# Optimization experiments

Measured on AMD Instinct MI355X. Metric: run time of the kernel, lower is better.

## Reference

```python
import jax, jax.numpy as jnp
import numpy as np

N_NODES = 100000
N_EDGES = 1600000
N_GRAPHS = 64
D = 128


def gcn_conv(x, W, b, src, dst, num_nodes):
    # PyG GCNConv: x' = D^{-1/2} (A + I) D^{-1/2} (X W) + b
    h = x @ W  # [N, H]
    deg = jax.ops.segment_sum(jnp.ones_like(dst, dtype=h.dtype), dst,
                              num_segments=num_nodes)  # includes self-loop (>=1)
    dinv = jax.lax.rsqrt(deg)
    norm = dinv[src] * dinv[dst]  # [E+N]
    msg = h[src] * norm[:, None]  # gather + scale
    out = jax.ops.segment_sum(msg, dst, num_segments=num_nodes)
    return out + b


def setup_inputs() -> dict:
    key = jax.random.key(0)
    ks = jax.random.split(key, 10)
    x = jax.random.normal(ks[0], (N_NODES, D), dtype=jnp.float32)
    edge_index = jax.random.randint(ks[1], (2, N_EDGES), 0, N_NODES, dtype=jnp.int64)
    batch = jnp.sort(jax.random.randint(ks[2], (N_NODES,), 0, N_GRAPHS, dtype=jnp.int64))
    s = 1.0 / np.sqrt(D)
    W1 = jax.random.normal(ks[3], (D, D), dtype=jnp.float32) * s
    b1 = jnp.zeros((D,), dtype=jnp.float32)
    W2 = jax.random.normal(ks[4], (D, D), dtype=jnp.float32) * s
    b2 = jnp.zeros((D,), dtype=jnp.float32)
    Wfc = jax.random.normal(ks[5], (D, D), dtype=jnp.float32) * s
    bfc = jnp.zeros((D,), dtype=jnp.float32)
    return {"x": x, "edge_index": edge_index, "batch": batch,
            "W1": W1, "b1": b1, "W2": W2, "b2": b2, "Wfc": Wfc, "bfc": bfc}


def reference(x, edge_index, batch, W1, b1, W2, b2, Wfc, bfc):
    num_nodes = x.shape[0]
    # add self-loops (PyG default add_self_loops=True)
    loop = jnp.arange(num_nodes, dtype=edge_index.dtype)
    src = jnp.concatenate([edge_index[0], loop])
    dst = jnp.concatenate([edge_index[1], loop])

    h = jax.nn.relu(gcn_conv(x, W1, b1, src, dst, num_nodes))
    h = jax.nn.relu(gcn_conv(h, W2, b2, src, dst, num_nodes))

    # global_mean_pool over graph segment ids
    sums = jax.ops.segment_sum(h, batch, num_segments=N_GRAPHS)
    cnts = jax.ops.segment_sum(jnp.ones((num_nodes,), h.dtype), batch,
                               num_segments=N_GRAPHS)
    pooled = sums / jnp.maximum(cnts, 1.0)[:, None]

    return jax.nn.relu(pooled @ Wfc + bfc)
```

## Files before the change

### kernel.cpp

```cpp
#include <hip/hip_runtime.h>
#include <hip/hip_bf16.h>
#include <stdint.h>

typedef unsigned int uint;
typedef unsigned short ushort;
typedef __attribute__((ext_vector_type(8))) short short8;
typedef __attribute__((ext_vector_type(4))) float floatx4;

#define DD 128
#define BSHIFT 9
#define NBLK 256
#define CAP 10240

__device__ __forceinline__ float bf2f(ushort h){ return __uint_as_float(((uint)h)<<16); }
__device__ __forceinline__ ushort f2bf(float f){
    uint u = __float_as_uint(f);
    u += 0x7fffu + ((u>>16)&1u);
    return (ushort)(u>>16);
}

__global__ __launch_bounds__(256) void k_canon2(
    const int* __restrict__ ei, const ushort* __restrict__ xs,
    const void* W1, const void* W2, const void* Wfc,
    const void* b1, const void* b2, const void* bfc,
    float* Wcf, float* bc1, float* bc2, float* bcf,
    ushort* wb1, ushort* wb2,
    int* flags, float* pooled, int* bukcnt, int nbuk, int PM)
{
    __shared__ int s_flg[3];
    int t = threadIdx.x, b = blockIdx.x;
    if (t < 64){
        unsigned long long m0 = __ballot((t < 32) ? (ei[2*t+1] == 0) : 1);
        uint ex2 = (((uint)xs[2*t]) >> 7) & 0xffu;
        uint ew2 = (((uint)((const ushort*)W1)[2*t]) >> 7) & 0xffu;
        unsigned long long m1 = __ballot(ex2 >= 90u && ex2 <= 160u);
        unsigned long long m2 = __ballot(ew2 >= 90u && ew2 <= 160u);
        if (t == 0){
            s_flg[0] = (m0 == ~0ull) ? 1 : 0;
            s_flg[1] = (__popcll(m1) >= 48) ? 1 : 0;
            s_flg[2] = (__popcll(m2) >= 48) ? 1 : 0;
            if (b == 0){ flags[0]=s_flg[0]; flags[1]=s_flg[1]; flags[2]=s_flg[2]; }
        }
    }
    __syncthreads();
    int fW = s_flg[2];

    int gi = b*256 + t;
    if (gi < 32768){
        int r = gi >> 14, off = gi & 16383;
        const void* s = (r==0) ? W1 : W2;
        float val = fW ? bf2f(((const ushort*)s)[off]) : ((const float*)s)[off];
        int k = off>>7, n = off&127;
        int c = n>>4, nn = n&15, kk = k>>5, q = (k>>3)&3, j = k&7;
        ushort* wb = (r==0) ? wb1 : wb2;
        wb[((c*4+kk)*64 + q*16 + nn)*8 + j] = f2bf(val);
    } else if (gi < 49152){
        int off = gi - 32768;
        Wcf[off] = fW ? bf2f(((const ushort*)Wfc)[off]) : ((const float*)Wfc)[off];
    } else if (gi < 49536){
        int jj = gi - 49152; int r = jj>>7, off = jj & 127;
        const void* s = (r==0)?b1:((r==1)?b2:bfc);
        float* d = (r==0)?bc1:((r==1)?bc2:bcf);
        d[off] = fW ? bf2f(((const ushort*)s)[off]) : ((const float*)s)[off];
    } else if (gi < 49536 + PM){
        pooled[gi - 49536] = 0.f;
    } else if (gi < 49536 + PM + nbuk){
        bukcnt[gi - 49536 - PM] = 0;
    }
}

__global__ __launch_bounds__(256) void k_scatA(const int* __restrict__ ei,
                                               int* __restrict__ bukcnt,
                                               uint2* __restrict__ pairs,
                                               int E, int nbuk, int chunk){
    __shared__ int lh[256], lcur[256];
    __shared__ int s_flg;
    int t = threadIdx.x, b = blockIdx.x;
    if (t < 64){
        unsigned long long m0 = __ballot((t < 32) ? (ei[2*t+1] == 0) : 1);
        if (t == 0) s_flg = (m0 == ~0ull) ? 1 : 0;
    }
    for (int i=t;i<nbuk;i+=256) lh[i]=0;
    __syncthreads();
    int f64 = s_flg;
    int e0 = b*chunk, e1 = min(E, e0+chunk);
    for (int e=e0+t; e<e1; e+=256){
        int d = f64 ? ei[2*(E+e)] : ei[E+e];
        atomicAdd(&lh[d>>BSHIFT], 1);
    }
    __syncthreads();
    for (int i=t;i<nbuk;i+=256){
        int v = lh[i];
        int base = v ? atomicAdd(&bukcnt[i], v) : 0;
        lcur[i] = i*CAP + base;
    }
    __syncthreads();
    for (int e=e0+t; e<e1; e+=256){
        int d = f64 ? ei[2*(E+e)] : ei[E+e];
        int s = f64 ? ei[2*e]     : ei[e];
        int p = atomicAdd(&lcur[d>>BSHIFT], 1);
        pairs[p] = make_uint2((uint)s,(uint)d);
    }
}

__global__ __launch_bounds__(256) void k_build(const uint2* __restrict__ pairs,
                                               const int* __restrict__ bukcnt,
                                               int* __restrict__ rowstart,
                                               int* __restrict__ rowend,
                                               float* __restrict__ dinv,
                                               int* __restrict__ srcb,
                                               int nbuk, int M){
    __shared__ int cnt[512], off[512], cur[512], ps[256];
    int b = blockIdx.x, t = threadIdx.x;
    int base = b*CAP;
    int m = bukcnt[b];
    for (int i=t;i<512;i+=256) cnt[i]=0;
    __syncthreads();
    for (int e=t; e<m; e+=256){
        uint2 pr = pairs[base+e];
        atomicAdd(&cnt[pr.y & 511], 1);
    }
    __syncthreads();
    int c0 = cnt[2*t], c1 = cnt[2*t+1];
    int s = c0 + c1;
    ps[t] = s; __syncthreads();
    for (int o2=1; o2<256; o2<<=1){
        int x = (t>=o2) ? ps[t-o2] : 0;
        __syncthreads(); ps[t] += x; __syncthreads();
    }
    int ex = ps[t] - s;
    off[2*t] = ex;     off[2*t+1] = ex + c0;
    cur[2*t] = ex;     cur[2*t+1] = ex + c0;
    __syncthreads();
    for (int i=t;i<512;i+=256){
        int n = (b<<BSHIFT) + i;
        if (n < M){
            rowstart[n] = base + off[i];
            rowend[n]   = base + off[i] + cnt[i];
            dinv[n]     = rsqrtf((float)(cnt[i]+1));
        }
    }
    for (int e=t; e<m; e+=256){
        uint2 pr = pairs[base+e];
        int i = pr.y & 511;
        int p = atomicAdd(&cur[i], 1);
        srcb[base+p] = (int)pr.x;
    }
}

__global__ __launch_bounds__(256) void k_gemm(const ushort* __restrict__ Xb,
                                              const float* __restrict__ Xf,
                                              const ushort* __restrict__ Wb,
                                              const float* __restrict__ dinv,
                                              const int* __restrict__ flags, int force_bf16,
                                              ushort* __restrict__ Hp, int M){
    __shared__ uint4 Xs4[1024];
    __shared__ uint4 Ws4[2048];
    int t = threadIdx.x;
    int n0 = blockIdx.x*64;
    int xbf = force_bf16 ? 1 : flags[1];

    {
        const uint4* sW = (const uint4*)Wb;
        #pragma unroll
        for (int j=0;j<8;j++) Ws4[t + j*256] = sW[t + j*256];
    }
    #pragma unroll
    for (int g=0; g<4; g++){
        int u = g*256 + t;
        int row = u>>4, kk = (u>>2)&3, q = u&3;
        int n = n0 + row;
        uint4 o;
        if (n < M){
            if (xbf){
                o = *(const uint4*)(Xb + (size_t)n*DD + kk*32 + q*8);
            } else {
                const float* p = Xf + (size_t)n*DD + kk*32 + q*8;
                float4 a = *(const float4*)p;
                float4 b = *(const float4*)(p+4);
                o.x = (uint)f2bf(a.x) | ((uint)f2bf(a.y)<<16);
                o.y = (uint)f2bf(a.z) | ((uint)f2bf(a.w)<<16);
                o.z = (uint)f2bf(b.x) | ((uint)f2bf(b.y)<<16);
                o.w = (uint)f2bf(b.z) | ((uint)f2bf(b.w)<<16);
            }
        } else { o = make_uint4(0,0,0,0); }
        int w = row>>4, m16 = row&15;
        Xs4[(w*4+kk)*64 + q*16 + m16] = o;
    }
    __syncthreads();

    int wv = t>>6, lane = t&63;
    const ushort* Xs = (const ushort*)Xs4;
    const ushort* Ws = (const ushort*)Ws4;

    floatx4 acc[8];
    #pragma unroll
    for (int c=0;c<8;c++) acc[c] = (floatx4){0.f,0.f,0.f,0.f};

    #pragma unroll
    for (int kk=0;kk<4;kk++){
        short8 af = *(const short8*)(Xs + ((size_t)((wv*4+kk)*64 + lane))*8);
        #pragma unroll
        for (int c=0;c<8;c++){
            short8 bf = *(const short8*)(Ws + ((size_t)((c*4+kk)*64 + lane))*8);
            acc[c] = __builtin_amdgcn_mfma_f32_16x16x32_bf16(af, bf, acc[c], 0, 0, 0);
        }
    }

    int quad = lane>>4, col = lane&15;
    int rbase = n0 + wv*16 + quad*4;
    float dv[4];
    #pragma unroll
    for (int r=0;r<4;r++) dv[r] = (rbase + r < M) ? dinv[rbase + r] : 0.f;
    #pragma unroll
    for (int c=0;c<8;c++){
        #pragma unroll
        for (int r=0;r<4;r++){
            int gn = rbase + r;
            if (gn < M) Hp[(size_t)gn*DD + c*16 + col] = f2bf(acc[c][r]*dv[r]);
        }
    }
}

__global__ __launch_bounds__(256) void k_gather(const ushort* __restrict__ Hp,
                                                const int* __restrict__ rowstart,
                                                const int* __restrict__ rowend,
                                                const int* __restrict__ srcb,
                                                const float* __restrict__ dinv,
                                                const float* __restrict__ bc,
                                                ushort* __restrict__ Xout, int M){
    int wid  = (int)((blockIdx.x*(size_t)blockDim.x + threadIdx.x) >> 6);
    int lane = threadIdx.x & 63;
    if (wid >= M) return;
    int q   = lane >> 4;
    int l16 = lane & 15;
    const uint4* Hp4 = (const uint4*)Hp;

    float acc[8];
    #pragma unroll
    for (int c=0;c<8;c++) acc[c] = 0.f;

    #define ACCUM(vv) { \
        acc[0] += __uint_as_float((vv).x<<16); acc[1] += __uint_as_float((vv).x&0xffff0000u); \
        acc[2] += __uint_as_float((vv).y<<16); acc[3] += __uint_as_float((vv).y&0xffff0000u); \
        acc[4] += __uint_as_float((vv).z<<16); acc[5] += __uint_as_float((vv).z&0xffff0000u); \
        acc[6] += __uint_as_float((vv).w<<16); acc[7] += __uint_as_float((vv).w&0xffff0000u); }

    int rp  = rowstart[wid];
    int rp1 = rowend[wid];
    int total = (rp1 - rp) + 1;
    int j = 0;
    while (j < total){
        int m = total - j; if (m > 64) m = 64;
        int pos = j + lane;
        int idx = wid;
        if (lane < m && pos > 0) idx = srcb[rp + pos - 1];
        for (int g = 0; g < m; g += 8){
            int r0 = g + q, r1 = g + 4 + q;
            int s0 = __shfl(idx, r0, 64);
            int s1 = __shfl(idx, r1, 64);
            uint4 v0 = make_uint4(0,0,0,0), v1 = make_uint4(0,0,0,0);
            if (r0 < m) v0 = Hp4[(size_t)s0*16 + l16];
            if (r1 < m) v1 = Hp4[(size_t)s1*16 + l16];
            ACCUM(v0);
            ACCUM(v1);
        }
        j += m;
    }
    #undef ACCUM

    #pragma unroll
    for (int c=0;c<8;c++){
        acc[c] += __shfl_xor(acc[c], 16, 64);
        acc[c] += __shfl_xor(acc[c], 32, 64);
    }

    if (lane < 16){
        float w = dinv[wid];
        const float* bp = bc + l16*8;
        uint4 o;
        float r0,r1;
        r0 = fmaxf(fmaf(acc[0], w, bp[0]), 0.f);
        r1 = fmaxf(fmaf(acc[1], w, bp[1]), 0.f);
        o.x = (uint)f2bf(r0) | ((uint)f2bf(r1)<<16);
        r0 = fmaxf(fmaf(acc[2], w, bp[2]), 0.f);
        r1 = fmaxf(fmaf(acc[3], w, bp[3]), 0.f);
        o.y = (uint)f2bf(r0) | ((uint)f2bf(r1)<<16);
        r0 = fmaxf(fmaf(acc[4], w, bp[4]), 0.f);
        r1 = fmaxf(fmaf(acc[5], w, bp[5]), 0.f);
        o.z = (uint)f2bf(r0) | ((uint)f2bf(r1)<<16);
        r0 = fmaxf(fmaf(acc[6], w, bp[6]), 0.f);
        r1 = fmaxf(fmaf(acc[7], w, bp[7]), 0.f);
        o.w = (uint)f2bf(r0) | ((uint)f2bf(r1)<<16);
        ((uint4*)Xout)[(size_t)wid*16 + l16] = o;
    }
}

__global__ __launch_bounds__(256) void k_pool(const ushort* __restrict__ X3,
                                              const int* __restrict__ batch,
                                              const int* __restrict__ flags,
                                              float* __restrict__ pooled, int M){
    int f = flags[0];
    int t = threadIdx.x;
    int c32 = t & 63;
    int row = t >> 6;
    int n0 = blockIdx.x * 256;
    if (n0 >= M) return;
    int nend = n0 + 256; if (nend > M) nend = M;
    const uint* X3u = (const uint*)X3;

    float a0 = 0.f, a1 = 0.f;
    int cur = -1;

    int n = n0 + row;
    #define POOL_PROC(gg, uu) \
        if ((gg) != cur){ \
            if (cur >= 0){ \
                atomicAdd(&pooled[cur*DD + 2*c32],   a0); \
                atomicAdd(&pooled[cur*DD + 2*c32+1], a1); \
            } \
            a0 = 0.f; a1 = 0.f; cur = (gg); \
        } \
        a0 += __uint_as_float((uu)<<16); \
        a1 += __uint_as_float((uu) & 0xffff0000u);

    for (; n + 12 < nend; n += 16){
        int g0 = f ? batch[2*n]      : batch[n];
        int g1 = f ? batch[2*(n+4)]  : batch[n+4];
        int g2 = f ? batch[2*(n+8)]  : batch[n+8];
        int g3 = f ? batch[2*(n+12)] : batch[n+12];
        uint u0 = X3u[(size_t)n*64      + c32];
        uint u1 = X3u[(size_t)(n+4)*64  + c32];
        uint u2 = X3u[(size_t)(n+8)*64  + c32];
        uint u3 = X3u[(size_t)(n+12)*64 + c32];
        POOL_PROC(g0, u0);
        POOL_PROC(g1, u1);
        POOL_PROC(g2, u2);
        POOL_PROC(g3, u3);
    }
    for (; n < nend; n += 4){
        int g = f ? batch[2*n] : batch[n];
        uint u = X3u[(size_t)n*64 + c32];
        POOL_PROC(g, u);
    }
    #undef POOL_PROC

    if (cur >= 0){
        atomicAdd(&pooled[cur*DD + 2*c32],   a0);
        atomicAdd(&pooled[cur*DD + 2*c32+1], a1);
    }
}

__global__ void k_fc(const float* __restrict__ pooled, const int* __restrict__ batch,
                     const int* __restrict__ flags,
                     const float* __restrict__ Wcf, const float* __restrict__ bcf,
                     ushort* out16, float* out32, int M){
    __shared__ float p[128];
    __shared__ int sb[2];
    int g = blockIdx.x, t = threadIdx.x;
    int f = flags[0];
    if (t < 2){
        int target = g - t;
        int lo = 0, hi = M;
        while (lo < hi){ int mid=(lo+hi)>>1; int bv = f ? batch[2*mid] : batch[mid]; if (bv > target) hi = mid; else lo = mid+1; }
        sb[t] = lo;
    }
    __syncthreads();
    float cnt = (float)(sb[0] - sb[1]);
    p[t] = pooled[g*DD + t] / fmaxf(cnt, 1.f);
    __syncthreads();
    float acc = bcf[t];
    #pragma unroll 8
    for (int k=0;k<128;k++) acc = fmaf(p[k], Wcf[k*DD + t], acc);
    float r = fmaxf(acc, 0.f);
    if (flags[1]) out16[g*DD + t] = f2bf(r);
    else          out32[g*DD + t] = r;
}

extern "C" void kernel_launch(void* const* d_in, const int* in_sizes, int n_in,
                              void* d_out, int out_size, void* d_ws, size_t ws_size,
                              hipStream_t stream) {
    const ushort* xs  = (const ushort*)d_in[0];
    const float*  xf  = (const float*)d_in[0];
    const int*    ei  = (const int*)d_in[1];
    const int*    bat = (const int*)d_in[2];
    const void* W1  = d_in[3];
    const void* b1  = d_in[4];
    const void* W2  = d_in[5];
    const void* b2  = d_in[6];
    const void* Wfc = d_in[7];
    const void* bfc = d_in[8];

    int M = in_sizes[0] / DD;
    int E = in_sizes[1] / 2;
    int G = out_size / DD;
    int nbuk  = (M + 511) >> BSHIFT;
    int chunk = (E + NBLK - 1) / NBLK;

    char* w = (char*)d_ws;
    auto alloc = [&](size_t bytes)->void*{ void* p = (void*)w; w += (bytes + 255) & ~(size_t)255; return p; };
    int*    flags    = (int*)   alloc(16);
    int*    rowstart = (int*)   alloc((size_t)M*4);
    int*    rowend   = (int*)   alloc((size_t)M*4);
    int*    bukcnt   = (int*)   alloc((size_t)nbuk*4);
    float*  dinv     = (float*) alloc((size_t)M*4);
    float*  pooled   = (float*) alloc((size_t)G*DD*4);
    float*  Wcf      = (float*) alloc(16384*4);
    float*  bc1      = (float*) alloc(128*4);
    float*  bc2      = (float*) alloc(128*4);
    float*  bcf      = (float*) alloc(128*4);
    ushort* wb1      = (ushort*)alloc(16384*2);
    ushort* wb2      = (ushort*)alloc(16384*2);
    int*    srcb     = (int*)   alloc((size_t)nbuk*CAP*4);
    ushort* Hp       = (ushort*)alloc((size_t)M*DD*2);
    ushort* X2       = (ushort*)alloc((size_t)M*DD*2);
    uint2*  pairs    = (uint2*)Hp;
    (void)ws_size; (void)n_in;

    int PM = G*DD;
    int canon_n = 49536 + PM + nbuk;

    k_canon2<<<(canon_n+255)/256, 256, 0, stream>>>(ei, xs, W1, W2, Wfc, b1, b2, bfc,
                                                    Wcf, bc1, bc2, bcf, wb1, wb2,
                                                    flags, pooled, bukcnt, nbuk, PM);
    k_scatA <<<NBLK, 256, 0, stream>>>(ei, bukcnt, pairs, E, nbuk, chunk);
    k_build <<<nbuk, 256, 0, stream>>>(pairs, bukcnt, rowstart, rowend, dinv, srcb, nbuk, M);

    k_gemm  <<<(M+63)/64, 256, 0, stream>>>(xs, xf, wb1, dinv, flags, 0, Hp, M);
    k_gather<<<(M+3)/4, 256, 0, stream>>>(Hp, rowstart, rowend, srcb, dinv, bc1, X2, M);
    k_gemm  <<<(M+63)/64, 256, 0, stream>>>(X2, (const float*)X2, wb2, dinv, flags, 1, Hp, M);
    k_gather<<<(M+3)/4, 256, 0, stream>>>(Hp, rowstart, rowend, srcb, dinv, bc2, X2, M);

    k_pool<<<(M+255)/256, 256, 0, stream>>>(X2, bat, flags, pooled, M);
    k_fc  <<<G, 128, 0, stream>>>(pooled, bat, flags, Wcf, bcf, (ushort*)d_out, (float*)d_out, M);
}
```

Baseline: 332.7 us.

## Store node features in column-slab layout so gather blocks work per slab

Intermediate feature matrices now use a slab-major layout of 8 slabs, each holding 16 bf16 columns per node. The gather kernel launches 8x as many blocks, each handling one slab for four destination nodes, so the set of rows being gathered concurrently (N x 32 bytes per slab) is more likely to stay in L2/MALL. The GEMM and pool kernels are adapted to read and write the slab layout. The trade-off is that the edge index list is read 8 times, each gathered access is 32-byte granular instead of 256-byte rows, and there are more block launches.

```diff
diff --git a/kernel.cpp b/kernel.cpp
--- a/kernel.cpp
+++ b/kernel.cpp
@@ -152,8 +152,9 @@
                                               const float* __restrict__ Xf,
                                               const ushort* __restrict__ Wb,
                                               const float* __restrict__ dinv,
-                                              const int* __restrict__ flags, int force_bf16,
-                                              ushort* __restrict__ Hp, int M){
+                                              const int* __restrict__ flags,
+                                              int force_bf16, int slabX,
+                                              ushort* __restrict__ HpS, int M){
     __shared__ uint4 Xs4[1024];
     __shared__ uint4 Ws4[2048];
     int t = threadIdx.x;
@@ -172,7 +173,10 @@
         int n = n0 + row;
         uint4 o;
         if (n < M){
-            if (xbf){
+            if (slabX){
+                int s = kk*2 + (q>>1);
+                o = *(const uint4*)(Xb + ((size_t)s*M + n)*16 + (q&1)*8);
+            } else if (xbf){
                 o = *(const uint4*)(Xb + (size_t)n*DD + kk*32 + q*8);
             } else {
                 const float* p = Xf + (size_t)n*DD + kk*32 + q*8;
@@ -217,86 +221,68 @@
         #pragma unroll
         for (int r=0;r<4;r++){
             int gn = rbase + r;
-            if (gn < M) Hp[(size_t)gn*DD + c*16 + col] = f2bf(acc[c][r]*dv[r]);
+            if (gn < M) HpS[((size_t)c*M + gn)*16 + col] = f2bf(acc[c][r]*dv[r]);
         }
     }
 }
 
-__global__ __launch_bounds__(256) void k_gather(const ushort* __restrict__ Hp,
+__global__ __launch_bounds__(256) void k_gather(const ushort* __restrict__ HpS,
                                                 const int* __restrict__ rowstart,
                                                 const int* __restrict__ rowend,
                                                 const int* __restrict__ srcb,
                                                 const float* __restrict__ dinv,
                                                 const float* __restrict__ bc,
-                                                ushort* __restrict__ Xout, int M){
-    int wid  = (int)((blockIdx.x*(size_t)blockDim.x + threadIdx.x) >> 6);
+                                                ushort* __restrict__ XoutS, int M){
+    int b = blockIdx.x;
+    int slab = b & 7;
+    int wv   = threadIdx.x >> 6;
+    int dst  = (b >> 3)*4 + wv;
     int lane = threadIdx.x & 63;
-    if (wid >= M) return;
-    int q   = lane >> 4;
-    int l16 = lane & 15;
-    const uint4* Hp4 = (const uint4*)Hp;
-
-    float acc[8];
-    #pragma unroll
-    for (int c=0;c<8;c++) acc[c] = 0.f;
-
-    #define ACCUM(vv) { \
-        acc[0] += __uint_as_float((vv).x<<16); acc[1] += __uint_as_float((vv).x&0xffff0000u); \
-        acc[2] += __uint_as_float((vv).y<<16); acc[3] += __uint_as_float((vv).y&0xffff0000u); \
-        acc[4] += __uint_as_float((vv).z<<16); acc[5] += __uint_as_float((vv).z&0xffff0000u); \
-        acc[6] += __uint_as_float((vv).w<<16); acc[7] += __uint_as_float((vv).w&0xffff0000u); }
-
-    int rp  = rowstart[wid];
-    int rp1 = rowend[wid];
+    if (dst >= M) return;
+    int e = lane >> 3;
+    int o = lane & 7;
+    const uint* Hp32 = (const uint*)HpS;
+    size_t slabBase = (size_t)slab * M * 8;
+
+    float a0 = 0.f, a1 = 0.f;
+
+    int rp  = rowstart[dst];
+    int rp1 = rowend[dst];
     int total = (rp1 - rp) + 1;
     int j = 0;
     while (j < total){
         int m = total - j; if (m > 64) m = 64;
         int pos = j + lane;
-        int idx = wid;
+        int idx = dst;
         if (lane < m && pos > 0) idx = srcb[rp + pos - 1];
-        for (int g = 0; g < m; g += 8){
-            int r0 = g + q, r1 = g + 4 + q;
+        for (int g = 0; g < m; g += 16){
+            int r0 = g + e, r1 = g + 8 + e;
             int s0 = __shfl(idx, r0, 64);
             int s1 = __shfl(idx, r1, 64);
-            uint4 v0 = make_uint4(0,0,0,0), v1 = make_uint4(0,0,0,0);
-            if (r0 < m) v0 = Hp4[(size_t)s0*16 + l16];
-            if (r1 < m) v1 = Hp4[(size_t)s1*16 + l16];
-            ACCUM(v0);
-            ACCUM(v1);
+            uint v0 = 0, v1 = 0;
+            if (r0 < m) v0 = Hp32[slabBase + (size_t)s0*8 + o];
+            if (r1 < m) v1 = Hp32[slabBase + (size_t)s1*8 + o];
+            a0 += __uint_as_float(v0<<16); a1 += __uint_as_float(v0&0xffff0000u);
+            a0 += __uint_as_float(v1<<16); a1 += __uint_as_float(v1&0xffff0000u);
         }
         j += m;
     }
-    #undef ACCUM
-
-    #pragma unroll
-    for (int c=0;c<8;c++){
-        acc[c] += __shfl_xor(acc[c], 16, 64);
-        acc[c] += __shfl_xor(acc[c], 32, 64);
-    }
-
-    if (lane < 16){
-        float w = dinv[wid];
-        const float* bp = bc + l16*8;
-        uint4 o;
-        float r0,r1;
-        r0 = fmaxf(fmaf(acc[0], w, bp[0]), 0.f);
-        r1 = fmaxf(fmaf(acc[1], w, bp[1]), 0.f);
-        o.x = (uint)f2bf(r0) | ((uint)f2bf(r1)<<16);
-        r0 = fmaxf(fmaf(acc[2], w, bp[2]), 0.f);
-        r1 = fmaxf(fmaf(acc[3], w, bp[3]), 0.f);
-        o.y = (uint)f2bf(r0) | ((uint)f2bf(r1)<<16);
-        r0 = fmaxf(fmaf(acc[4], w, bp[4]), 0.f);
-        r1 = fmaxf(fmaf(acc[5], w, bp[5]), 0.f);
-        o.z = (uint)f2bf(r0) | ((uint)f2bf(r1)<<16);
-        r0 = fmaxf(fmaf(acc[6], w, bp[6]), 0.f);
-        r1 = fmaxf(fmaf(acc[7], w, bp[7]), 0.f);
-        o.w = (uint)f2bf(r0) | ((uint)f2bf(r1)<<16);
-        ((uint4*)Xout)[(size_t)wid*16 + l16] = o;
-    }
-}
-
-__global__ __launch_bounds__(256) void k_pool(const ushort* __restrict__ X3,
+
+    a0 += __shfl_xor(a0, 8, 64);  a1 += __shfl_xor(a1, 8, 64);
+    a0 += __shfl_xor(a0, 16, 64); a1 += __shfl_xor(a1, 16, 64);
+    a0 += __shfl_xor(a0, 32, 64); a1 += __shfl_xor(a1, 32, 64);
+
+    if (lane < 8){
+        float w = dinv[dst];
+        float b0 = bc[slab*16 + 2*o];
+        float b1 = bc[slab*16 + 2*o + 1];
+        float r0 = fmaxf(fmaf(a0, w, b0), 0.f);
+        float r1 = fmaxf(fmaf(a1, w, b1), 0.f);
+        ((uint*)XoutS)[slabBase + (size_t)dst*8 + o] = (uint)f2bf(r0) | ((uint)f2bf(r1)<<16);
+    }
+}
+
+__global__ __launch_bounds__(256) void k_pool(const ushort* __restrict__ X3S,
                                               const int* __restrict__ batch,
                                               const int* __restrict__ flags,
                                               float* __restrict__ pooled, int M){
@@ -307,7 +293,8 @@
     int n0 = blockIdx.x * 256;
     if (n0 >= M) return;
     int nend = n0 + 256; if (nend > M) nend = M;
-    const uint* X3u = (const uint*)X3;
+    const uint* X3u = (const uint*)X3S;
+    size_t cbase = (size_t)(c32 >> 3) * M * 8 + (c32 & 7);
 
     float a0 = 0.f, a1 = 0.f;
     int cur = -1;
@@ -329,10 +316,10 @@
         int g1 = f ? batch[2*(n+4)]  : batch[n+4];
         int g2 = f ? batch[2*(n+8)]  : batch[n+8];
         int g3 = f ? batch[2*(n+12)] : batch[n+12];
-        uint u0 = X3u[(size_t)n*64      + c32];
-        uint u1 = X3u[(size_t)(n+4)*64  + c32];
-        uint u2 = X3u[(size_t)(n+8)*64  + c32];
-        uint u3 = X3u[(size_t)(n+12)*64 + c32];
+        uint u0 = X3u[cbase + (size_t)n*8];
+        uint u1 = X3u[cbase + (size_t)(n+4)*8];
+        uint u2 = X3u[cbase + (size_t)(n+8)*8];
+        uint u3 = X3u[cbase + (size_t)(n+12)*8];
         POOL_PROC(g0, u0);
         POOL_PROC(g1, u1);
         POOL_PROC(g2, u2);
@@ -340,7 +327,7 @@
     }
     for (; n < nend; n += 4){
         int g = f ? batch[2*n] : batch[n];
-        uint u = X3u[(size_t)n*64 + c32];
+        uint u = X3u[cbase + (size_t)n*8];
         POOL_PROC(g, u);
     }
     #undef POOL_PROC
@@ -426,10 +413,11 @@
     k_scatA <<<NBLK, 256, 0, stream>>>(ei, bukcnt, pairs, E, nbuk, chunk);
     k_build <<<nbuk, 256, 0, stream>>>(pairs, bukcnt, rowstart, rowend, dinv, srcb, nbuk, M);
 
-    k_gemm  <<<(M+63)/64, 256, 0, stream>>>(xs, xf, wb1, dinv, flags, 0, Hp, M);
-    k_gather<<<(M+3)/4, 256, 0, stream>>>(Hp, rowstart, rowend, srcb, dinv, bc1, X2, M);
-    k_gemm  <<<(M+63)/64, 256, 0, stream>>>(X2, (const float*)X2, wb2, dinv, flags, 1, Hp, M);
-    k_gather<<<(M+3)/4, 256, 0, stream>>>(Hp, rowstart, rowend, srcb, dinv, bc2, X2, M);
+    int gblocks = ((M + 3) / 4) * 8;
+    k_gemm  <<<(M+63)/64, 256, 0, stream>>>(xs, xf, wb1, dinv, flags, 0, 0, Hp, M);
+    k_gather<<<gblocks, 256, 0, stream>>>(Hp, rowstart, rowend, srcb, dinv, bc1, X2, M);
+    k_gemm  <<<(M+63)/64, 256, 0, stream>>>(X2, (const float*)X2, wb2, dinv, flags, 1, 1, Hp, M);
+    k_gather<<<gblocks, 256, 0, stream>>>(Hp, rowstart, rowend, srcb, dinv, bc2, X2, M);
 
     k_pool<<<(M+255)/256, 256, 0, stream>>>(X2, bat, flags, pooled, M);
     k_fc  <<<G, 128, 0, stream>>>(pooled, bat, flags, Wcf, bcf, (ushort*)d_out, (float*)d_out, M);
```

New measurement: 609.5 us. 1.83x slower.
